# Kernel tuning notes

Measured on AMD Instinct MI355X. Metric: run time of the kernel, lower is better.

## Reference

```python
import jax, jax.numpy as jnp
import numpy as np

N_SEQ = 100_000
N_LAB = 64
E_CON = 1_600_000
D_IN = 128; D_HID = 128; BEL_OUT = 64; INC_OUT = 128
BN_EPS = 1e-5


def setup_inputs() -> dict:
    key = jax.random.key(0)
    ks = jax.random.split(key, 16)
    def W(k, i, o):
        return jax.random.normal(k, (i, o), jnp.float32) / np.float32(np.sqrt(i))
    return {
        "x_seq": jax.random.normal(ks[0], (N_SEQ, D_IN), jnp.float32),
        "x_label": jax.random.normal(ks[1], (N_LAB, D_IN), jnp.float32),
        "W1_bel": W(ks[2], D_IN, D_HID), "b1_bel": jnp.zeros((D_HID,), jnp.float32),
        "W1_inc": W(ks[3], D_IN, D_HID), "b1_inc": jnp.zeros((D_HID,), jnp.float32),
        "W1_con": W(ks[4], D_IN, D_HID), "b1_con": jnp.zeros((D_HID,), jnp.float32),
        "g1s": jnp.ones((D_HID,), jnp.float32), "beta1s": jnp.zeros((D_HID,), jnp.float32),
        "g1l": jnp.ones((D_HID,), jnp.float32), "beta1l": jnp.zeros((D_HID,), jnp.float32),
        "W2_bel": W(ks[5], D_HID, BEL_OUT), "b2_bel": jnp.zeros((BEL_OUT,), jnp.float32),
        "W2_inc": W(ks[6], D_HID, INC_OUT), "b2_inc": jnp.zeros((INC_OUT,), jnp.float32),
        "W2_con": W(ks[7], D_HID, INC_OUT), "b2_con": jnp.zeros((INC_OUT,), jnp.float32),
        "g2s": jnp.ones((INC_OUT,), jnp.float32), "beta2s": jnp.zeros((INC_OUT,), jnp.float32),
        "g2l": jnp.ones((BEL_OUT,), jnp.float32), "beta2l": jnp.zeros((BEL_OUT,), jnp.float32),
        "bel_label": jax.random.randint(ks[8], (N_SEQ,), 0, N_LAB),
        "con_src": jax.random.randint(ks[9], (E_CON,), 0, N_SEQ),
        "con_dst": jax.random.randint(ks[10], (E_CON,), 0, N_SEQ),
    }


def _inv_sqrt_deg(deg):
    # DGL norm='both': deg^{-1/2}, zero-degree nodes get 0
    return jnp.where(deg > 0, jax.lax.rsqrt(jnp.maximum(deg, 1.0)), 0.0)


def _gconv(x_src, src, dst, n_dst, W, b):
    # DGL GraphConv: y = D_dst^{-1/2} A D_src^{-1/2} x W + b
    n_src = x_src.shape[0]
    ones = jnp.ones(src.shape, x_src.dtype)
    deg_out = jax.ops.segment_sum(ones, src, num_segments=n_src)
    deg_in = jax.ops.segment_sum(ones, dst, num_segments=n_dst)
    xs = x_src * _inv_sqrt_deg(deg_out)[:, None]
    agg = jax.ops.segment_sum(xs[src], dst, num_segments=n_dst)  # [n_dst, d]
    agg = agg * _inv_sqrt_deg(deg_in)[:, None]
    return agg @ W + b


def _bn(x, g, b):
    # BatchNorm1d, training mode: biased variance, eps=1e-5
    m = jnp.mean(x, axis=0)
    v = jnp.mean(jnp.square(x - m), axis=0)
    return (x - m) * jax.lax.rsqrt(v + BN_EPS) * g + b


def _hetero_layer(h_seq, h_lab, bel_label, con_src, con_dst, Wb, bb, Wi, bi, Wc, bc):
    seq_idx = jnp.arange(h_seq.shape[0])
    # belongs_to: sequence -> label
    lab = _gconv(h_seq, seq_idx, bel_label, h_lab.shape[0], Wb, bb)
    # including: label -> sequence; connected_to: sequence -> sequence
    inc = _gconv(h_lab, bel_label, seq_idx, h_seq.shape[0], Wi, bi)
    con = _gconv(h_seq, con_src, con_dst, h_seq.shape[0], Wc, bc)
    # HeteroGraphConv aggregate='mean' over relations per dst type
    seq = 0.5 * (inc + con)
    return jax.nn.relu(seq), jax.nn.relu(lab)


def reference(x_seq, x_label,
              W1_bel, b1_bel, W1_inc, b1_inc, W1_con, b1_con,
              g1s, beta1s, g1l, beta1l,
              W2_bel, b2_bel, W2_inc, b2_inc, W2_con, b2_con,
              g2s, beta2s, g2l, beta2l,
              bel_label, con_src, con_dst):
    h_s, h_l = _hetero_layer(x_seq, x_label, bel_label, con_src, con_dst,
                             W1_bel, b1_bel, W1_inc, b1_inc, W1_con, b1_con)
    h_s = _bn(h_s, g1s, beta1s)
    h_l = _bn(h_l, g1l, beta1l)
    h_s, h_l = _hetero_layer(h_s, h_l, bel_label, con_src, con_dst,
                             W2_bel, b2_bel, W2_inc, b2_inc, W2_con, b2_con)
    h_s = _bn(h_s, g2s, beta2s)
    h_l = _bn(h_l, g2l, beta2l)
    return (h_s, h_l)
```

## Files before the change

kernel.cpp:

```cpp
#include <hip/hip_runtime.h>
#include <hip/hip_bf16.h>

#define NSEQ 100000
#define NLAB 64
#define ECON 1600000
#define D 128
#define BN_EPS 1e-5f

#define NB 196
#define BW 512
#define BCAP 10240
#define EPB 4096
#define NPART 32
#define RPB 4096

typedef unsigned int uint32;
typedef __attribute__((ext_vector_type(8))) short bf16x8;
typedef __attribute__((ext_vector_type(4))) float f32x4;

__device__ __forceinline__ void atomAddF(float* p, float v) {
  unsafeAtomicAdd(p, v);
}
__device__ __forceinline__ float blo(uint32 u) {
  union { uint32 u; float f; } c; c.u = u << 16; return c.f;
}
__device__ __forceinline__ float bhi(uint32 u) {
  union { uint32 u; float f; } c; c.u = u & 0xFFFF0000u; return c.f;
}
__device__ __forceinline__ unsigned short f2b(float f) {
  __hip_bfloat16 h = __float2bfloat16(f);
  union { __hip_bfloat16 h; unsigned short s; } c; c.h = h; return c.s;
}

__global__ __launch_bounds__(256) void k_label_hist(const int* __restrict__ lab, int* cnt) {
  __shared__ int h[NLAB];
  if (threadIdx.x < NLAB) h[threadIdx.x] = 0;
  __syncthreads();
  for (int i = blockIdx.x * 256 + threadIdx.x; i < NSEQ; i += gridDim.x * 256)
    atomicAdd(&h[lab[i]], 1);
  __syncthreads();
  if (threadIdx.x < NLAB) atomicAdd(&cnt[threadIdx.x], h[threadIdx.x]);
}

__global__ __launch_bounds__(256) void k_binA(const int* __restrict__ src,
                                              const int* __restrict__ dst,
                                              int* deg_out, int* bucket_cnt,
                                              uint32* __restrict__ bpair) {
  __shared__ int hist[NB];
  __shared__ int base[NB];
  int t = threadIdx.x;
  for (int i = t; i < NB; i += 256) hist[i] = 0;
  __syncthreads();
  int e0 = blockIdx.x * EPB;
  int e1 = min(e0 + EPB, ECON);
  for (int e = e0 + t; e < e1; e += 256) {
    int d = dst[e];
    atomicAdd(&hist[d >> 9], 1);
    atomicAdd(&deg_out[src[e]], 1);
  }
  __syncthreads();
  for (int i = t; i < NB; i += 256) {
    int c = hist[i];
    base[i] = (c > 0) ? atomicAdd(&bucket_cnt[i], c) : 0;
    hist[i] = 0;
  }
  __syncthreads();
  for (int e = e0 + t; e < e1; e += 256) {
    int d = dst[e];
    int b = d >> 9;
    int p = base[b] + atomicAdd(&hist[b], 1);
    bpair[b * BCAP + p] = (uint32)src[e] | ((uint32)(d & (BW - 1)) << 17);
  }
}

__global__ __launch_bounds__(256) void k_bscan(const int* __restrict__ bucket_cnt,
                                               int* __restrict__ bbase,
                                               const int* __restrict__ cnt_lab,
                                               float* __restrict__ dinv_cnt,
                                               int* __restrict__ lab_base,
                                               int* __restrict__ lab_cursor) {
  int t = threadIdx.x;
  if (t == 0) {
    int acc = 0;
    for (int i = 0; i < NB; ++i) { bbase[i] = acc; acc += bucket_cnt[i]; }
    bbase[NB] = acc;
  }
  if (t == 1) {
    int acc = 0;
    for (int i = 0; i < NLAB; ++i) {
      lab_base[i] = acc; lab_cursor[i] = acc; acc += cnt_lab[i];
    }
    lab_base[NLAB] = acc;
  }
  if (t < NLAB) { int c = cnt_lab[t]; dinv_cnt[t] = c > 0 ? rsqrtf((float)c) : 0.f; }
}

__global__ __launch_bounds__(256) void k_binB(const uint32* __restrict__ bpair,
                                              const int* __restrict__ bucket_cnt,
                                              const int* __restrict__ bbase,
                                              const int* deg_out,
                                              int* __restrict__ off,
                                              float* __restrict__ dinv_in,
                                              float* dinv_out,
                                              int* __restrict__ esrc) {
  __shared__ int deg[BW];
  __shared__ int loff[BW];
  __shared__ int cursor[BW];
  __shared__ int wsum[4];
  int b = blockIdx.x;
  int t = threadIdx.x;
  int cnt = bucket_cnt[b];
  int gbase = bbase[b];
  const uint32* bp = &bpair[(size_t)b * BCAP];
  deg[t] = 0; deg[t + 256] = 0;
  cursor[t] = 0; cursor[t + 256] = 0;
  __syncthreads();
  for (int i = t; i < cnt; i += 256)
    atomicAdd(&deg[bp[i] >> 17], 1);
  __syncthreads();
  int d0 = deg[2 * t], d1 = deg[2 * t + 1];
  int ps = d0 + d1;
  int lane = t & 63, w = t >> 6;
  int v = ps;
  #pragma unroll
  for (int o = 1; o < 64; o <<= 1) { int n = __shfl_up(v, o); if (lane >= o) v += n; }
  if (lane == 63) wsum[w] = v;
  __syncthreads();
  int wbase = 0;
  for (int i = 0; i < w; ++i) wbase += wsum[i];
  int excl = wbase + v - ps;
  loff[2 * t] = excl;
  loff[2 * t + 1] = excl + d0;
  __syncthreads();
  #pragma unroll
  for (int k = 0; k < 2; ++k) {
    int j = t + k * 256;
    int node = b * BW + j;
    if (node < NSEQ) {
      int dg = deg[j];
      off[node] = gbase + loff[j];
      dinv_in[node] = dg > 0 ? rsqrtf((float)dg) : 0.f;
      int dgo = deg_out[node];
      dinv_out[node] = dgo > 0 ? rsqrtf((float)dgo) : 0.f;
    }
  }
  if (b == NB - 1 && t == 0) off[NSEQ] = ECON;
  for (int i = t; i < cnt; i += 256) {
    uint32 pk = bp[i];
    int dl = pk >> 17;
    int p = gbase + loff[dl] + atomicAdd(&cursor[dl], 1);
    esrc[p] = (int)(pk & 0x1FFFF);
  }
}

__global__ __launch_bounds__(256) void k_lab_scatter(const int* __restrict__ lab,
                                                     int* lab_cursor,
                                                     int* __restrict__ lab_sorted) {
  __shared__ int hist[NLAB], base[NLAB];
  int t = threadIdx.x;
  if (t < NLAB) hist[t] = 0;
  __syncthreads();
  int r0 = blockIdx.x * RPB, r1 = min(r0 + RPB, NSEQ);
  for (int r = r0 + t; r < r1; r += 256) atomicAdd(&hist[lab[r]], 1);
  __syncthreads();
  if (t < NLAB) {
    int c = hist[t];
    base[t] = (c > 0) ? atomicAdd(&lab_cursor[t], c) : 0;
    hist[t] = 0;
  }
  __syncthreads();
  for (int r = r0 + t; r < r1; r += 256) {
    int l = lab[r];
    int p = base[l] + atomicAdd(&hist[l], 1);
    lab_sorted[p] = r;
  }
}

__global__ __launch_bounds__(256) void k_lab_agg(const uint32* __restrict__ xb,
                                                 const int* __restrict__ lab_sorted,
                                                 const int* __restrict__ lab_base,
                                                 float* __restrict__ lab_agg) {
  __shared__ float accs[4][D];
  int t = threadIdx.x;
  int l = blockIdx.x >> 3, p = blockIdx.x & 7;
  int w = t >> 6, cp = t & 63;
  int i0 = lab_base[l], i1 = lab_base[l + 1];
  float ax = 0.f, ay = 0.f;
  for (int i = i0 + p * 4 + w; i < i1; i += 32) {
    int r = lab_sorted[i];
    uint32 u = xb[r * 64 + cp];
    ax += blo(u); ay += bhi(u);
  }
  accs[w][2 * cp] = ax;
  accs[w][2 * cp + 1] = ay;
  __syncthreads();
  if (w == 0) {
    float s0 = accs[0][2 * cp] + accs[1][2 * cp] + accs[2][2 * cp] + accs[3][2 * cp];
    float s1 = accs[0][2 * cp + 1] + accs[1][2 * cp + 1] + accs[2][2 * cp + 1] + accs[3][2 * cp + 1];
    atomAddF(&lab_agg[l * D + 2 * cp], s0);
    atomAddF(&lab_agg[l * D + 2 * cp + 1], s1);
  }
}

__global__ __launch_bounds__(256) void k_cast(const float* __restrict__ x,
                                              uint32* __restrict__ xb) {
  int i = blockIdx.x * 256 + threadIdx.x;
  if (i >= NSEQ * D / 4) return;
  float4 v = ((const float4*)x)[i];
  uint32 u0 = (uint32)f2b(v.x) | ((uint32)f2b(v.y) << 16);
  uint32 u1 = (uint32)f2b(v.z) | ((uint32)f2b(v.w) << 16);
  ((uint2*)xb)[i] = make_uint2(u0, u1);
}

__global__ __launch_bounds__(256) void k_prep_w(const float* __restrict__ W1,
                                                const float* __restrict__ W2,
                                                short* __restrict__ wT1,
                                                short* __restrict__ wT2) {
  int i = blockIdx.x * 256 + threadIdx.x;
  if (i < 16384) {
    int k = i >> 7, c = i & 127;
    wT1[c * 128 + k] = (short)f2b(W1[i]);
  } else if (i < 32768) {
    int j = i - 16384;
    int k = j >> 7, c = j & 127;
    wT2[c * 128 + k] = (short)f2b(W2[j]);
  }
}

__global__ __launch_bounds__(256) void k_mm(
    const float* __restrict__ A, const float* __restrict__ rowscale,
    const float* __restrict__ W, const float* __restrict__ bias,
    float* __restrict__ out, int ncol, int relu) {
  __shared__ float sA[4 * D];
  int tid = threadIdx.x;
  int rows_pb = 256 / ncol;
  int row0 = blockIdx.x * rows_pb;
  int nload = rows_pb * D;
  for (int i = tid; i < nload; i += 256) {
    int r = row0 + (i >> 7);
    float s = rowscale ? rowscale[r] : 1.f;
    sA[i] = A[r * D + (i & 127)] * s;
  }
  __syncthreads();
  int j = tid & (ncol - 1);
  int r = tid / ncol;
  const float* a = &sA[r * D];
  const float* w = &W[j];
  float acc0 = 0.f, acc1 = 0.f, acc2 = 0.f, acc3 = 0.f;
  #pragma unroll 4
  for (int k = 0; k < D; k += 4) {
    acc0 = fmaf(a[k + 0], w[(k + 0) * ncol], acc0);
    acc1 = fmaf(a[k + 1], w[(k + 1) * ncol], acc1);
    acc2 = fmaf(a[k + 2], w[(k + 2) * ncol], acc2);
    acc3 = fmaf(a[k + 3], w[(k + 3) * ncol], acc3);
  }
  float s = (acc0 + acc1) + (acc2 + acc3);
  if (bias) s += bias[j];
  if (relu) s = fmaxf(s, 0.f);
  out[(row0 + r) * ncol + j] = s;
}

__global__ __launch_bounds__(256) void k_label_bn(
    const float* __restrict__ pre,
    const float* __restrict__ g, const float* __restrict__ beta,
    float* __restrict__ out, int ncol) {
  __shared__ float psum[256], psq[256];
  __shared__ float sa[128], sc[128];
  int tid = threadIdx.x;
  int ngrp = 256 / ncol;
  int grp = tid / ncol;
  int col = tid & (ncol - 1);
  float s = 0.f, q = 0.f;
  for (int r = grp; r < NLAB; r += ngrp) {
    float v = pre[r * ncol + col];
    s += v; q += v * v;
  }
  psum[tid] = s; psq[tid] = q;
  __syncthreads();
  if (tid < ncol) {
    float S = 0.f, Q = 0.f;
    for (int gi = 0; gi < ngrp; ++gi) { S += psum[gi * ncol + tid]; Q += psq[gi * ncol + tid]; }
    float m = S * (1.f / NLAB);
    float v = Q * (1.f / NLAB) - m * m;
    float a = rsqrtf(v + BN_EPS) * g[tid];
    sa[tid] = a; sc[tid] = beta[tid] - m * a;
  }
  __syncthreads();
  for (int i = tid; i < NLAB * ncol; i += 256) {
    int c = i & (ncol - 1);
    out[i] = pre[i] * sa[c] + sc[c];
  }
}

__global__ __launch_bounds__(256) void k_con_agg_bf(
    const uint32* __restrict__ xb, const int* __restrict__ esrc,
    const int* __restrict__ off,
    const float* __restrict__ dinv_out, const float* __restrict__ dinv_in,
    uint32* __restrict__ outb) {
  int wid = (blockIdx.x * 256 + threadIdx.x) >> 6;
  int lane = threadIdx.x & 63;
  if (wid >= NSEQ) return;
  int e0 = off[wid], e1 = off[wid + 1];
  float ax = 0.f, ay = 0.f;
  int e = e0;
  for (; e + 3 < e1; e += 4) {
    int s0 = esrc[e], s1 = esrc[e + 1], s2 = esrc[e + 2], s3 = esrc[e + 3];
    float w0 = dinv_out[s0], w1 = dinv_out[s1], w2 = dinv_out[s2], w3 = dinv_out[s3];
    uint32 u0 = xb[s0 * 64 + lane];
    uint32 u1 = xb[s1 * 64 + lane];
    uint32 u2 = xb[s2 * 64 + lane];
    uint32 u3 = xb[s3 * 64 + lane];
    ax += blo(u0) * w0 + blo(u1) * w1 + blo(u2) * w2 + blo(u3) * w3;
    ay += bhi(u0) * w0 + bhi(u1) * w1 + bhi(u2) * w2 + bhi(u3) * w3;
  }
  for (; e < e1; ++e) {
    int s0 = esrc[e];
    float w0 = dinv_out[s0];
    uint32 u0 = xb[s0 * 64 + lane];
    ax += blo(u0) * w0;
    ay += bhi(u0) * w0;
  }
  float di = dinv_in[wid];
  uint32 p = (uint32)f2b(ax * di) | ((uint32)f2b(ay * di) << 16);
  outb[wid * 64 + lane] = p;
}

template <int OUTBF>
__global__ __launch_bounds__(256) void k_gemm_mfma(
    const short* __restrict__ aggbf,
    const short* __restrict__ wT,
    const float* __restrict__ b_con,
    const float* __restrict__ y_inc,
    const float* __restrict__ b_inc,
    const float* __restrict__ dinv_cnt,
    const int* __restrict__ bel,
    float* __restrict__ outF,
    short* __restrict__ outB,
    float* __restrict__ statsP) {
  __shared__ short sW[128 * 136];
  __shared__ float csum[D], csq[D];
  int t = threadIdx.x;
  {
    const uint4* src = (const uint4*)wT;
    for (int i = t; i < 2048; i += 256) {
      int row = i >> 4, part = i & 15;
      *(uint4*)&sW[row * 136 + part * 8] = src[i];
    }
  }
  if (t < D) { csum[t] = 0.f; csq[t] = 0.f; }
  int w = t >> 6, l = t & 63;
  int lr = l & 15, lg = l >> 4;
  int row0 = blockIdx.x * 64 + w * 16;
  bf16x8 afrag[4];
  {
    int arow = min(row0 + lr, NSEQ - 1);
    const short* ab = aggbf + arow * 128 + lg * 8;
    #pragma unroll
    for (int kt = 0; kt < 4; ++kt)
      afrag[kt] = *(const bf16x8*)(ab + kt * 32);
  }
  __syncthreads();
  f32x4 acc[8];
  #pragma unroll
  for (int ct = 0; ct < 8; ++ct) {
    f32x4 a = {0.f, 0.f, 0.f, 0.f};
    const short* wb = &sW[(ct * 16 + lr) * 136 + lg * 8];
    #pragma unroll
    for (int kt = 0; kt < 4; ++kt) {
      bf16x8 bfr = *(const bf16x8*)(wb + kt * 32);
      a = __builtin_amdgcn_mfma_f32_16x16x32_bf16(afrag[kt], bfr, a, 0, 0, 0);
    }
    acc[ct] = a;
  }
  int belr[4]; float dcv[4]; int rowv[4];
  #pragma unroll
  for (int r = 0; r < 4; ++r) {
    int gr = row0 + lg * 4 + r;
    rowv[r] = gr;
    int cl = min(gr, NSEQ - 1);
    belr[r] = bel[cl];
    dcv[r] = dinv_cnt[belr[r]];
  }
  #pragma unroll
  for (int ct = 0; ct < 8; ++ct) {
    int col = ct * 16 + lr;
    float bc = b_con[col], bi = b_inc[col];
    float s = 0.f, q = 0.f;
    #pragma unroll
    for (int r = 0; r < 4; ++r) {
      if (rowv[r] < NSEQ) {
        float o = acc[ct][r] + bc + fmaf(dcv[r], y_inc[belr[r] * D + col], bi);
        o = fmaxf(0.5f * o, 0.f);
        if (OUTBF) outB[rowv[r] * D + col] = (short)f2b(o);
        else       outF[rowv[r] * D + col] = o;
        s += o; q += o * o;
      }
    }
    s += __shfl_xor(s, 16); s += __shfl_xor(s, 32);
    q += __shfl_xor(q, 16); q += __shfl_xor(q, 32);
    if (lg == 0) {
      atomicAdd(&csum[col], s);
      atomicAdd(&csq[col], q);
    }
  }
  __syncthreads();
  float* sp = statsP + (blockIdx.x & (NPART - 1)) * 256;
  if (t < D) {
    atomAddF(&sp[t], csum[t]);
    atomAddF(&sp[D + t], csq[t]);
  }
}

__global__ __launch_bounds__(256) void k_bn_apply_bf(
    const uint32* __restrict__ pre, const float* __restrict__ statsP,
    const float* __restrict__ g, const float* __restrict__ beta,
    uint32* __restrict__ xb) {
  int t = threadIdx.x;
  int w = t >> 6, cp = t & 63;
  int c0 = 2 * cp, c1 = 2 * cp + 1;
  float s0 = 0.f, q0 = 0.f, s1 = 0.f, q1 = 0.f;
  #pragma unroll
  for (int k = 0; k < NPART; ++k) {
    const float* sp = statsP + k * 256;
    s0 += sp[c0]; q0 += sp[128 + c0];
    s1 += sp[c1]; q1 += sp[128 + c1];
  }
  const float invN = 1.f / (float)NSEQ;
  float m0 = s0 * invN, m1 = s1 * invN;
  float a0 = rsqrtf(q0 * invN - m0 * m0 + BN_EPS) * g[c0];
  float a1 = rsqrtf(q1 * invN - m1 * m1 + BN_EPS) * g[c1];
  float cc0 = beta[c0] - m0 * a0;
  float cc1 = beta[c1] - m1 * a1;
  for (int r = blockIdx.x * 4 + w; r < NSEQ; r += gridDim.x * 4) {
    uint32 u = pre[r * 64 + cp];
    float v0 = blo(u) * a0 + cc0;
    float v1 = bhi(u) * a1 + cc1;
    xb[r * 64 + cp] = (uint32)f2b(v0) | ((uint32)f2b(v1) << 16);
  }
}

__global__ __launch_bounds__(256) void k_bn_apply2(
    float* __restrict__ buf, const float* __restrict__ statsP,
    const float* __restrict__ g, const float* __restrict__ beta) {
  int t = threadIdx.x;
  int w = t >> 6, cp = t & 63;
  int c0 = 2 * cp, c1 = 2 * cp + 1;
  float s0 = 0.f, q0 = 0.f, s1 = 0.f, q1 = 0.f;
  #pragma unroll
  for (int k = 0; k < NPART; ++k) {
    const float* sp = statsP + k * 256;
    s0 += sp[c0]; q0 += sp[128 + c0];
    s1 += sp[c1]; q1 += sp[128 + c1];
  }
  const float invN = 1.f / (float)NSEQ;
  float m0 = s0 * invN, m1 = s1 * invN;
  float a0 = rsqrtf(q0 * invN - m0 * m0 + BN_EPS) * g[c0];
  float a1 = rsqrtf(q1 * invN - m1 * m1 + BN_EPS) * g[c1];
  float cc0 = beta[c0] - m0 * a0;
  float cc1 = beta[c1] - m1 * a1;
  for (int r = blockIdx.x * 4 + w; r < NSEQ; r += gridDim.x * 4) {
    float2 v = ((float2*)buf)[r * 64 + cp];
    v.x = v.x * a0 + cc0;
    v.y = v.y * a1 + cc1;
    ((float2*)buf)[r * 64 + cp] = v;
  }
}

extern "C" void kernel_launch(void* const* d_in, const int* in_sizes, int n_in,
                              void* d_out, int out_size, void* d_ws, size_t ws_size,
                              hipStream_t stream) {
  const float* x_seq   = (const float*)d_in[0];
  const float* x_label = (const float*)d_in[1];
  const float* W1_bel  = (const float*)d_in[2];
  const float* b1_bel  = (const float*)d_in[3];
  const float* W1_inc  = (const float*)d_in[4];
  const float* b1_inc  = (const float*)d_in[5];
  const float* W1_con  = (const float*)d_in[6];
  const float* b1_con  = (const float*)d_in[7];
  const float* g1s     = (const float*)d_in[8];
  const float* beta1s  = (const float*)d_in[9];
  const float* g1l     = (const float*)d_in[10];
  const float* beta1l  = (const float*)d_in[11];
  const float* W2_bel  = (const float*)d_in[12];
  const float* b2_bel  = (const float*)d_in[13];
  const float* W2_inc  = (const float*)d_in[14];
  const float* b2_inc  = (const float*)d_in[15];
  const float* W2_con  = (const float*)d_in[16];
  const float* b2_con  = (const float*)d_in[17];
  const float* g2s     = (const float*)d_in[18];
  const float* beta2s  = (const float*)d_in[19];
  const float* g2l     = (const float*)d_in[20];
  const float* beta2l  = (const float*)d_in[21];
  const int* bel       = (const int*)d_in[22];
  const int* con_src   = (const int*)d_in[23];
  const int* con_dst   = (const int*)d_in[24];
  float* out = (float*)d_out;

  char* ws = (char*)d_ws;
  short*  aggbf    = (short*) (ws);
  short*  h1pre    = (short*) (ws + 25600000);
  uint32* bpair    = (uint32*)(ws + 32000000);
  int*    esrc     = (int*)   (ws + 51200000);
  int*    deg_out    = (int*)  (ws + 57600000);
  int*    cnt_lab    = (int*)  (ws + 58000000);
  int*    bucket_cnt = (int*)  (ws + 58001024);
  float*  statsP1    = (float*)(ws + 58002048);
  float*  statsP2    = (float*)(ws + 58034816);
  float*  lab_agg1   = (float*)(ws + 58067584);
  float*  lab_agg2   = (float*)(ws + 58100352);
  float*  dinv_in    = (float*)(ws + 58133120);
  float*  dinv_cnt   = (float*)(ws + 58533120);
  int*    bbase      = (int*)  (ws + 58533376);
  int*    off        = (int*)  (ws + 58534400);
  float*  y_inc1     = (float*)(ws + 58934528);
  float*  y_inc2     = (float*)(ws + 58967296);
  float*  h_l1       = (float*)(ws + 59000064);
  short*  wT1        = (short*)(ws + 59032832);
  short*  wT2        = (short*)(ws + 59065600);
  int*    lab_base   = (int*)  (ws + 59098368);
  int*    lab_cursor = (int*)  (ws + 59099392);
  int*    lab_sorted = (int*)  (ws + 59100416);

  float* dinv_out = (float*)deg_out;
  uint32* xb = (uint32*)out;
  float* belp1 = (float*)ws;
  float* belp2 = (float*)ws;

  hipMemsetAsync(ws + 57600000, 0, 533120, stream);

  k_label_hist <<<256, 256, 0, stream>>>(bel, cnt_lab);
  k_binA       <<<(ECON + EPB - 1) / EPB, 256, 0, stream>>>(con_src, con_dst,
                                                            deg_out, bucket_cnt, bpair);
  k_bscan      <<<1, 256, 0, stream>>>(bucket_cnt, bbase, cnt_lab, dinv_cnt,
                                       lab_base, lab_cursor);
  k_binB       <<<NB, 256, 0, stream>>>(bpair, bucket_cnt, bbase, deg_out,
                                        off, dinv_in, dinv_out, esrc);
  k_lab_scatter<<<(NSEQ + RPB - 1) / RPB, 256, 0, stream>>>(bel, lab_cursor, lab_sorted);
  k_cast       <<<(NSEQ * D / 4 + 255) / 256, 256, 0, stream>>>(x_seq, xb);
  k_prep_w     <<<128, 256, 0, stream>>>(W1_con, W2_con, wT1, wT2);

  k_lab_agg    <<<NLAB * 8, 256, 0, stream>>>(xb, lab_sorted, lab_base, lab_agg1);
  k_mm         <<<32, 256, 0, stream>>>(x_label, nullptr, W1_inc, nullptr, y_inc1, 128, 0);
  k_mm         <<<32, 256, 0, stream>>>(lab_agg1, dinv_cnt, W1_bel, b1_bel, belp1, 128, 1);
  k_label_bn   <<<1, 256, 0, stream>>>(belp1, g1l, beta1l, h_l1, 128);
  k_con_agg_bf <<<NSEQ / 4, 256, 0, stream>>>(xb, esrc, off, dinv_out, dinv_in,
                                              (uint32*)aggbf);
  k_gemm_mfma<1><<<(NSEQ + 63) / 64, 256, 0, stream>>>(
                   aggbf, wT1, b1_con, y_inc1, b1_inc, dinv_cnt, bel,
                   nullptr, h1pre, statsP1);
  k_bn_apply_bf<<<1024, 256, 0, stream>>>((uint32*)h1pre, statsP1, g1s, beta1s, xb);

  k_lab_agg    <<<NLAB * 8, 256, 0, stream>>>(xb, lab_sorted, lab_base, lab_agg2);
  k_mm         <<<32, 256, 0, stream>>>(h_l1, nullptr, W2_inc, nullptr, y_inc2, 128, 0);
  k_mm         <<<16, 256, 0, stream>>>(lab_agg2, dinv_cnt, W2_bel, b2_bel, belp2, 64, 1);
  k_label_bn   <<<1, 256, 0, stream>>>(belp2, g2l, beta2l, out + (size_t)NSEQ * D, 64);
  k_con_agg_bf <<<NSEQ / 4, 256, 0, stream>>>(xb, esrc, off, dinv_out, dinv_in,
                                              (uint32*)aggbf);
  k_gemm_mfma<0><<<(NSEQ + 63) / 64, 256, 0, stream>>>(
                   aggbf, wT2, b2_con, y_inc2, b2_inc, dinv_cnt, bel,
                   out, nullptr, statsP2);
  k_bn_apply2  <<<1024, 256, 0, stream>>>(out, statsP2, g2s, beta2s);
}
```

Before: 489.7 us.

## Replace global out-degree atomics with bucketed source binning and LDS-staged coalesced writes

The edge binning kernel no longer does a global atomicAdd per edge for out-degree. It also bins source ids into per-512-node buckets and computes degrees in a new per-bucket kernel using shared-memory atomics. Both destination and source records are first sorted locally in LDS per block, then written to global memory contiguously per bucket, which should coalesce the scattered writes. The cost is more LDS use per block (about 32KB), lower occupancy, an extra kernel launch and an extra pass over the 2-byte source records.

```diff
diff --git a/kernel.cpp b/kernel.cpp
--- a/kernel.cpp
+++ b/kernel.cpp
@@ -15,6 +15,7 @@
 #define RPB 4096
 
 typedef unsigned int uint32;
+typedef unsigned short ushort;
 typedef __attribute__((ext_vector_type(8))) short bf16x8;
 typedef __attribute__((ext_vector_type(4))) float f32x4;
 
@@ -44,32 +45,52 @@
 
 __global__ __launch_bounds__(256) void k_binA(const int* __restrict__ src,
                                               const int* __restrict__ dst,
-                                              int* deg_out, int* bucket_cnt,
-                                              uint32* __restrict__ bpair) {
-  __shared__ int hist[NB];
-  __shared__ int base[NB];
-  int t = threadIdx.x;
-  for (int i = t; i < NB; i += 256) hist[i] = 0;
+                                              int* bucket_cnt, int* sbucket_cnt,
+                                              uint32* __restrict__ bpair,
+                                              ushort* __restrict__ spair) {
+  __shared__ uint32 recD[EPB];
+  __shared__ ushort recS[EPB];
+  __shared__ unsigned char bidD[EPB];
+  __shared__ unsigned char bidS[EPB];
+  __shared__ int histD[NB], histS[NB], loffD[NB], loffS[NB], gbD[NB], gbS[NB];
+  int t = threadIdx.x;
+  for (int i = t; i < NB; i += 256) { histD[i] = 0; histS[i] = 0; }
   __syncthreads();
   int e0 = blockIdx.x * EPB;
   int e1 = min(e0 + EPB, ECON);
   for (int e = e0 + t; e < e1; e += 256) {
-    int d = dst[e];
-    atomicAdd(&hist[d >> 9], 1);
-    atomicAdd(&deg_out[src[e]], 1);
-  }
+    atomicAdd(&histD[dst[e] >> 9], 1);
+    atomicAdd(&histS[src[e] >> 9], 1);
+  }
+  __syncthreads();
+  if (t == 0) { int a = 0; for (int i = 0; i < NB; ++i) { loffD[i] = a; a += histD[i]; } }
+  if (t == 1) { int a = 0; for (int i = 0; i < NB; ++i) { loffS[i] = a; a += histS[i]; } }
   __syncthreads();
   for (int i = t; i < NB; i += 256) {
-    int c = hist[i];
-    base[i] = (c > 0) ? atomicAdd(&bucket_cnt[i], c) : 0;
-    hist[i] = 0;
+    int c = histD[i]; gbD[i] = c ? atomicAdd(&bucket_cnt[i], c) : 0; histD[i] = 0;
+    int cs = histS[i]; gbS[i] = cs ? atomicAdd(&sbucket_cnt[i], cs) : 0; histS[i] = 0;
   }
   __syncthreads();
   for (int e = e0 + t; e < e1; e += 256) {
-    int d = dst[e];
+    int s = src[e], d = dst[e];
     int b = d >> 9;
-    int p = base[b] + atomicAdd(&hist[b], 1);
-    bpair[b * BCAP + p] = (uint32)src[e] | ((uint32)(d & (BW - 1)) << 17);
+    int p = loffD[b] + atomicAdd(&histD[b], 1);
+    recD[p] = (uint32)s | ((uint32)(d & (BW - 1)) << 17);
+    bidD[p] = (unsigned char)b;
+    int bs = s >> 9;
+    int q = loffS[bs] + atomicAdd(&histS[bs], 1);
+    recS[q] = (ushort)(s & (BW - 1));
+    bidS[q] = (unsigned char)bs;
+  }
+  __syncthreads();
+  int n = e1 - e0;
+  for (int i = t; i < n; i += 256) {
+    int b = bidD[i];
+    bpair[(size_t)b * BCAP + gbD[b] + (i - loffD[b])] = recD[i];
+  }
+  for (int i = t; i < n; i += 256) {
+    int b = bidS[i];
+    spair[(size_t)b * BCAP + gbS[b] + (i - loffS[b])] = recS[i];
   }
 }
 
@@ -98,10 +119,8 @@
 __global__ __launch_bounds__(256) void k_binB(const uint32* __restrict__ bpair,
                                               const int* __restrict__ bucket_cnt,
                                               const int* __restrict__ bbase,
-                                              const int* deg_out,
                                               int* __restrict__ off,
                                               float* __restrict__ dinv_in,
-                                              float* dinv_out,
                                               int* __restrict__ esrc) {
   __shared__ int deg[BW];
   __shared__ int loff[BW];
@@ -140,8 +159,6 @@
       int dg = deg[j];
       off[node] = gbase + loff[j];
       dinv_in[node] = dg > 0 ? rsqrtf((float)dg) : 0.f;
-      int dgo = deg_out[node];
-      dinv_out[node] = dgo > 0 ? rsqrtf((float)dgo) : 0.f;
     }
   }
   if (b == NB - 1 && t == 0) off[NSEQ] = ECON;
@@ -150,6 +167,28 @@
     int dl = pk >> 17;
     int p = gbase + loff[dl] + atomicAdd(&cursor[dl], 1);
     esrc[p] = (int)(pk & 0x1FFFF);
+  }
+}
+
+__global__ __launch_bounds__(256) void k_binBS(const ushort* __restrict__ spair,
+                                               const int* __restrict__ sbucket_cnt,
+                                               float* __restrict__ dinv_out) {
+  __shared__ int deg[BW];
+  int b = blockIdx.x, t = threadIdx.x;
+  int cnt = sbucket_cnt[b];
+  deg[t] = 0; deg[t + 256] = 0;
+  __syncthreads();
+  const ushort* sp = &spair[(size_t)b * BCAP];
+  for (int i = t; i < cnt; i += 256) atomicAdd(&deg[sp[i]], 1);
+  __syncthreads();
+  #pragma unroll
+  for (int k = 0; k < 2; ++k) {
+    int j = t + k * 256;
+    int node = b * BW + j;
+    if (node < NSEQ) {
+      int dg = deg[j];
+      dinv_out[node] = dg > 0 ? rsqrtf((float)dg) : 0.f;
+    }
   }
 }
 
@@ -500,41 +539,44 @@
   short*  aggbf    = (short*) (ws);
   short*  h1pre    = (short*) (ws + 25600000);
   uint32* bpair    = (uint32*)(ws + 32000000);
+  ushort* spair    = (ushort*)(ws + 40028160);
   int*    esrc     = (int*)   (ws + 51200000);
-  int*    deg_out    = (int*)  (ws + 57600000);
-  int*    cnt_lab    = (int*)  (ws + 58000000);
-  int*    bucket_cnt = (int*)  (ws + 58001024);
-  float*  statsP1    = (float*)(ws + 58002048);
-  float*  statsP2    = (float*)(ws + 58034816);
-  float*  lab_agg1   = (float*)(ws + 58067584);
-  float*  lab_agg2   = (float*)(ws + 58100352);
-  float*  dinv_in    = (float*)(ws + 58133120);
-  float*  dinv_cnt   = (float*)(ws + 58533120);
-  int*    bbase      = (int*)  (ws + 58533376);
-  int*    off        = (int*)  (ws + 58534400);
-  float*  y_inc1     = (float*)(ws + 58934528);
-  float*  y_inc2     = (float*)(ws + 58967296);
-  float*  h_l1       = (float*)(ws + 59000064);
-  short*  wT1        = (short*)(ws + 59032832);
-  short*  wT2        = (short*)(ws + 59065600);
-  int*    lab_base   = (int*)  (ws + 59098368);
-  int*    lab_cursor = (int*)  (ws + 59099392);
-  int*    lab_sorted = (int*)  (ws + 59100416);
-
-  float* dinv_out = (float*)deg_out;
+  float*  dinv_out = (float*) (ws + 57600000);
+  int*    cnt_lab     = (int*)  (ws + 58000000);
+  int*    bucket_cnt  = (int*)  (ws + 58001024);
+  int*    sbucket_cnt = (int*)  (ws + 58002048);
+  float*  statsP1     = (float*)(ws + 58003072);
+  float*  statsP2     = (float*)(ws + 58035840);
+  float*  lab_agg1    = (float*)(ws + 58068608);
+  float*  lab_agg2    = (float*)(ws + 58101376);
+  float*  dinv_in    = (float*)(ws + 58134144);
+  float*  dinv_cnt   = (float*)(ws + 58534144);
+  int*    bbase      = (int*)  (ws + 58534400);
+  int*    off        = (int*)  (ws + 58535424);
+  float*  y_inc1     = (float*)(ws + 58935552);
+  float*  y_inc2     = (float*)(ws + 58968320);
+  float*  h_l1       = (float*)(ws + 59001088);
+  short*  wT1        = (short*)(ws + 59033856);
+  short*  wT2        = (short*)(ws + 59066624);
+  int*    lab_base   = (int*)  (ws + 59099392);
+  int*    lab_cursor = (int*)  (ws + 59100416);
+  int*    lab_sorted = (int*)  (ws + 59101440);
+
   uint32* xb = (uint32*)out;
   float* belp1 = (float*)ws;
   float* belp2 = (float*)ws;
 
-  hipMemsetAsync(ws + 57600000, 0, 533120, stream);
+  hipMemsetAsync(ws + 58000000, 0, 134144, stream);
 
   k_label_hist <<<256, 256, 0, stream>>>(bel, cnt_lab);
   k_binA       <<<(ECON + EPB - 1) / EPB, 256, 0, stream>>>(con_src, con_dst,
-                                                            deg_out, bucket_cnt, bpair);
+                                                            bucket_cnt, sbucket_cnt,
+                                                            bpair, spair);
   k_bscan      <<<1, 256, 0, stream>>>(bucket_cnt, bbase, cnt_lab, dinv_cnt,
                                        lab_base, lab_cursor);
-  k_binB       <<<NB, 256, 0, stream>>>(bpair, bucket_cnt, bbase, deg_out,
-                                        off, dinv_in, dinv_out, esrc);
+  k_binB       <<<NB, 256, 0, stream>>>(bpair, bucket_cnt, bbase,
+                                        off, dinv_in, esrc);
+  k_binBS      <<<NB, 256, 0, stream>>>(spair, sbucket_cnt, dinv_out);
   k_lab_scatter<<<(NSEQ + RPB - 1) / RPB, 256, 0, stream>>>(bel, lab_cursor, lab_sorted);
   k_cast       <<<(NSEQ * D / 4 + 255) / 256, 256, 0, stream>>>(x_seq, xb);
   k_prep_w     <<<128, 256, 0, stream>>>(W1_con, W2_con, wT1, wT2);
```

Measured after the change: 455.8 us. -6.9%, faster.
